# Optimization experiments

Hardware: AMD Instinct MI355X
Metric: run time of the kernel (lower is better)

Reference implementation:

```python
import jax, jax.numpy as jnp
import numpy as np

B, N = 8, 2048
DIN, DH, DE = 32, 64, 64
R = 3          # number_relations
L = 3          # num_layers -> 1 first + 1 block + 1 last
PRED_IN = DH * (L - 1) + DE  # concat: 64*2 + 64 = 192
EPS_BN = 1e-5
EPS_NORM = 1e-12


def setup_inputs() -> dict:
    key = jax.random.key(0)
    ks = jax.random.split(key, 12)
    x = jax.random.normal(ks[0], (B, N, DIN), jnp.float32)
    # relation labels in {0..R}; 0 = no edge, 1..R = relation type
    relation = jax.random.randint(ks[1], (B, N, N), 0, R + 1).astype(jnp.int32)
    # adjacency is the 0/1 edge indicator (float), as the torch code treats it
    adj = (relation > 0).astype(jnp.float32)
    s = 0.05
    w_first = jax.random.normal(ks[2], (R, DIN, DH), jnp.float32) * s
    b_first = jnp.zeros((DH,), jnp.float32)
    w_block = jax.random.normal(ks[3], (R, DH, DH), jnp.float32) * s
    b_block = jnp.zeros((DH,), jnp.float32)
    w_last = jax.random.normal(ks[4], (R, DH, DE), jnp.float32) * s
    b_last = jnp.zeros((DE,), jnp.float32)
    w_map = jax.random.normal(ks[5], (PRED_IN, DE), jnp.float32) * s
    b_map = jnp.zeros((DE,), jnp.float32)
    return {"x": x, "relation": relation, "adj": adj,
            "w_first": w_first, "b_first": b_first,
            "w_block": w_block, "b_block": b_block,
            "w_last": w_last, "b_last": b_last,
            "w_map": w_map, "b_map": b_map}


def _graph_conv(x, rel, W, b):
    # rel: [B,N,N] (int labels or float adjacency); W: [R, din, dout]
    y = jnp.zeros((x.shape[0], x.shape[1], W.shape[2]), x.dtype)
    for i in range(R):  # fixed, small relation count
        mask = (rel == (i + 1)).astype(x.dtype)            # [B,N,N]
        h = jnp.einsum('bij,bjd->bid', mask, x)            # masked aggregation
        y = y + jnp.einsum('bid,de->bie', h, W[i])
    y = y + b
    # F.normalize(p=2, dim=2): v / max(||v||, eps)
    nrm = jnp.sqrt(jnp.sum(y * y, axis=2, keepdims=True))
    return y / jnp.maximum(nrm, EPS_NORM)


def _apply_bn(x):
    # fresh BatchNorm1d(N) in training mode, affine weight=1/bias=0:
    # normalize over (batch, feature) per node index, biased variance
    mean = jnp.mean(x, axis=(0, 2), keepdims=True)
    var = jnp.mean(jnp.square(x - mean), axis=(0, 2), keepdims=True)
    return (x - mean) * jax.lax.rsqrt(var + EPS_BN)


def reference(x, relation, adj, w_first, b_first, w_block, b_block,
              w_last, b_last, w_map, b_map):
    # conv_first uses `relation`
    h = _apply_bn(jax.nn.relu(_graph_conv(x, relation, w_first, b_first)))
    out_all = [jnp.max(h, axis=1)]
    # conv_block and conv_last are (faithfully) called with `adj` as relation
    h = _apply_bn(jax.nn.relu(_graph_conv(h, adj, w_block, b_block)))
    out_all.append(jnp.max(h, axis=1))
    h = _graph_conv(h, adj, w_last, b_last)
    out_all.append(jnp.max(h, axis=1))
    output = jnp.concatenate(out_all, axis=1)        # [B, PRED_IN]
    ypred = output @ w_map + b_map                   # map_model Linear
    return (output, ypred)
```

## Files before the change

kernel.cpp:

```cpp
#include <hip/hip_runtime.h>


#define NN 2048
#define PLANE_W 1048576L

typedef short short8 __attribute__((ext_vector_type(8)));
typedef float floatx4 __attribute__((ext_vector_type(4)));

__device__ __forceinline__ unsigned short f2bf(float x) {
  unsigned u = __float_as_uint(x);
  u += 0x7FFFu + ((u >> 16) & 1u);
  return (unsigned short)(u >> 16);
}

__device__ void dev_xw_first(char* smemc, int u, int tid,
                             const float* __restrict__ x,
                             const float* __restrict__ w,
                             unsigned short* __restrict__ xws) {
  float* xs = (float*)smemc;
  float* wsh = (float*)(smemc + 64 * 33 * 4);
  const int jc = u & 31, b = (u >> 5) & 7, r = u >> 8;
  const int j0 = jc * 64;
  for (int idx = tid; idx < 64 * 32; idx += 256) {
    int row = idx >> 5, f = idx & 31;
    xs[row * 33 + f] = x[((long)b * NN + j0 + row) * 32 + f];
    wsh[idx] = w[r * 2048 + idx];
  }
  __syncthreads();
  const int j = tid & 63, g = tid >> 6;
  const int k = j0 + j;
  const int kblk = k >> 5, kq = (k >> 3) & 3, kj = k & 7;
  unsigned short* dst =
      xws + (((long)(r * 8 + b) * 64 + kblk) * 4 + g) * 512 + kj;
  float xr[32];
#pragma unroll
  for (int f = 0; f < 32; ++f) xr[f] = xs[j * 33 + f];
#pragma unroll
  for (int ii = 0; ii < 16; ++ii) {
    float acc = 0.f;
#pragma unroll
    for (int f = 0; f < 32; ++f) acc += xr[f] * wsh[f * 64 + g * 16 + ii];
    dst[(kq * 16 + ii) * 8] = f2bf(acc);
  }
  __syncthreads();
}

__global__ __launch_bounds__(256) void k_pack_xw1(const int* __restrict__ rel,
                                                  unsigned* __restrict__ planes,
                                                  unsigned* __restrict__ UP,
                                                  const float* __restrict__ x,
                                                  const float* __restrict__ w,
                                                  unsigned short* __restrict__ xws) {
  __shared__ __align__(16) char smem[16640];
  const int bid = blockIdx.x, tid = threadIdx.x;
  if (bid < 768) dev_xw_first(smem, bid, tid, x, w, xws);
  for (long t = (long)bid * 256 + tid; t < 1048576L; t += 4096L * 256) {
    int w32 = (int)(t & 63);
    long bi = t >> 6;
    const int4* rp = (const int4*)(rel + bi * NN + w32 * 32);
    unsigned m0 = 0, m1 = 0, m2 = 0;
#pragma unroll
    for (int c = 0; c < 8; ++c) {
      int4 v = rp[c];
      int vv[4] = {v.x, v.y, v.z, v.w};
#pragma unroll
      for (int j = 0; j < 4; ++j) {
        unsigned b1 = 1u << (c * 4 + j);
        m0 |= (vv[j] == 1) ? b1 : 0u;
        m1 |= (vv[j] == 2) ? b1 : 0u;
        m2 |= (vv[j] == 3) ? b1 : 0u;
      }
    }
    long o = bi * 64 + w32;
    planes[o] = m0;
    planes[PLANE_W + o] = m1;
    planes[2 * PLANE_W + o] = m2;
    UP[o] = m0 | m1 | m2;
  }
}

template <int NREL, bool RELU, bool POOL3>
__global__ __launch_bounds__(512) void k_gemm8(
    const unsigned* __restrict__ planes, const unsigned short* __restrict__ xws,
    const float* __restrict__ bias, float* __restrict__ Hout,
    float* __restrict__ part3) {
  constexpr int SMEM = (NREL * 8448 > 16640) ? NREL * 8448 : 16640;
  __shared__ __align__(16) char smem[SMEM];
  unsigned* mw = (unsigned*)smem;
  floatx4* cb = (floatx4*)smem;
  const int bid = blockIdx.x;
  const int b = bid & 7, it = bid >> 3;
  const int tid = threadIdx.x;
  const int wave = tid >> 6, lane = tid & 63;
  const int m = lane & 15, kq = lane >> 4;
  const int i0 = it * 64;

  floatx4 acc[4][4];
#pragma unroll
  for (int rs = 0; rs < 4; ++rs)
#pragma unroll
    for (int t = 0; t < 4; ++t) acc[rs][t] = floatx4{0, 0, 0, 0};

  for (int chunk = 0; chunk < 2; ++chunk) {
    for (int idx = tid; idx < NREL * 2048; idx += 512) {
      int p = idx >> 11, rem = idx & 2047, row = rem >> 5, w = rem & 31;
      long g = ((long)b * NN + i0 + row) * 64 + chunk * 32 + w;
      unsigned v = (NREL == 3) ? planes[(long)p * PLANE_W + g] : planes[g];
      mw[(p * 64 + row) * 33 + w] = v;
    }
    __syncthreads();
#pragma unroll
    for (int j = 0; j < 4; ++j) {
      const int kk = j * 8 + wave;
      const int kblk = chunk * 32 + kk;
#pragma unroll
      for (int p = 0; p < NREL; ++p) {
        const unsigned short* bb =
            xws + ((long)(p * 8 + b) * 64 + kblk) * 2048 + lane * 8;
        short8 bf0 = *(const short8*)(bb);
        short8 bf1 = *(const short8*)(bb + 512);
        short8 bf2 = *(const short8*)(bb + 1024);
        short8 bf3 = *(const short8*)(bb + 1536);
#pragma unroll
        for (int rs = 0; rs < 4; ++rs) {
          unsigned word = mw[(p * 64 + rs * 16 + m) * 33 + kk];
          unsigned byte = (word >> (kq * 8)) & 0xffu;
          unsigned pp = byte | (byte << 15);
          union {
            unsigned uu[4];
            short8 s8;
          } fr;
          fr.uu[0] = (pp & 0x00010001u) * 0x3F80u;
          fr.uu[1] = (pp & 0x00040004u) * 0x0FE0u;
          fr.uu[2] = (pp & 0x00100010u) * 0x03F8u;
          fr.uu[3] = (pp & 0x00400040u) * 0x00FEu;
          acc[rs][0] = __builtin_amdgcn_mfma_f32_16x16x32_bf16(fr.s8, bf0,
                                                              acc[rs][0], 0, 0, 0);
          acc[rs][1] = __builtin_amdgcn_mfma_f32_16x16x32_bf16(fr.s8, bf1,
                                                              acc[rs][1], 0, 0, 0);
          acc[rs][2] = __builtin_amdgcn_mfma_f32_16x16x32_bf16(fr.s8, bf2,
                                                              acc[rs][2], 0, 0, 0);
          acc[rs][3] = __builtin_amdgcn_mfma_f32_16x16x32_bf16(fr.s8, bf3,
                                                              acc[rs][3], 0, 0, 0);
        }
      }
    }
    __syncthreads();
  }

  for (int k = 7; k >= 1; --k) {
    if (wave == k) {
      if (k == 7) {
#pragma unroll
        for (int rs = 0; rs < 4; ++rs)
#pragma unroll
          for (int t = 0; t < 4; ++t) cb[(rs * 4 + t) * 64 + lane] = acc[rs][t];
      } else {
#pragma unroll
        for (int rs = 0; rs < 4; ++rs)
#pragma unroll
          for (int t = 0; t < 4; ++t) {
            floatx4 v = cb[(rs * 4 + t) * 64 + lane];
            cb[(rs * 4 + t) * 64 + lane] = v + acc[rs][t];
          }
      }
    }
    __syncthreads();
  }
  if (wave == 0) {
#pragma unroll
    for (int rs = 0; rs < 4; ++rs)
#pragma unroll
      for (int t = 0; t < 4; ++t) acc[rs][t] += cb[(rs * 4 + t) * 64 + lane];
    float bv[4];
#pragma unroll
    for (int t = 0; t < 4; ++t) bv[t] = bias[t * 16 + m];
    float pmt[4] = {-3.4e38f, -3.4e38f, -3.4e38f, -3.4e38f};
#pragma unroll
    for (int rs = 0; rs < 4; ++rs) {
      float ss[4];
#pragma unroll
      for (int reg = 0; reg < 4; ++reg) {
#pragma unroll
        for (int t = 0; t < 4; ++t) acc[rs][t][reg] += bv[t];
        ss[reg] = acc[rs][0][reg] * acc[rs][0][reg] +
                  acc[rs][1][reg] * acc[rs][1][reg] +
                  acc[rs][2][reg] * acc[rs][2][reg] +
                  acc[rs][3][reg] * acc[rs][3][reg];
#pragma unroll
        for (int off = 1; off <= 8; off <<= 1)
          ss[reg] += __shfl_xor(ss[reg], off);
        ss[reg] = 1.0f / fmaxf(sqrtf(ss[reg]), 1e-12f);
      }
#pragma unroll
      for (int t = 0; t < 4; ++t) {
#pragma unroll
        for (int reg = 0; reg < 4; ++reg) {
          float o = acc[rs][t][reg] * ss[reg];
          if (RELU) o = fmaxf(o, 0.0f);
          if (POOL3)
            pmt[t] = fmaxf(pmt[t], o);
          else
            Hout[((long)b * NN + i0 + rs * 16 + kq * 4 + reg) * 64 + t * 16 + m] = o;
        }
      }
    }
    if (POOL3) {
#pragma unroll
      for (int t = 0; t < 4; ++t) {
        pmt[t] = fmaxf(pmt[t], __shfl_xor(pmt[t], 16));
        pmt[t] = fmaxf(pmt[t], __shfl_xor(pmt[t], 32));
      }
      if (kq == 0) {
#pragma unroll
        for (int t = 0; t < 4; ++t)
          part3[((long)b * 32 + it) * 64 + t * 16 + m] = pmt[t];
      }
    }
  }
}

__global__ __launch_bounds__(256) void k_xwh_bn(const float* __restrict__ H,
                                                const float* __restrict__ w,
                                                unsigned short* __restrict__ xws,
                                                float* __restrict__ PP) {
  __shared__ float hs[64 * 65];
  __shared__ float wsh[64 * 64];
  __shared__ float sm[64], srs[64];
  const int bid = blockIdx.x, tid = threadIdx.x;
  const int jc = bid & 31, b = bid >> 5;
  const int j0 = jc * 64;
  {
    const int n = tid >> 2, q = tid & 3;
    float s1 = 0.f, s2 = 0.f;
#pragma unroll
    for (int bb = 0; bb < 8; ++bb) {
      const float4* hp =
          (const float4*)(H + ((long)bb * NN + j0 + n) * 64 + q * 16);
#pragma unroll
      for (int c = 0; c < 4; ++c) {
        float4 v = hp[c];
        s1 += v.x + v.y + v.z + v.w;
        s2 += v.x * v.x + v.y * v.y + v.z * v.z + v.w * v.w;
      }
    }
    s1 += __shfl_xor(s1, 1);
    s2 += __shfl_xor(s2, 1);
    s1 += __shfl_xor(s1, 2);
    s2 += __shfl_xor(s2, 2);
    if (q == 0) {
      float mean = s1 * (1.0f / 512.0f);
      float var = fmaxf(s2 * (1.0f / 512.0f) - mean * mean, 0.0f);
      sm[n] = mean;
      srs[n] = rsqrtf(var + 1e-5f);
    }
  }
  __syncthreads();
  for (int idx = tid; idx < 4096; idx += 256) {
    int row = idx >> 6, f = idx & 63;
    float v = H[((long)b * NN + j0 + row) * 64 + f];
    hs[row * 65 + f] = (v - sm[row]) * srs[row];
    wsh[idx] = w[idx];
  }
  __syncthreads();
  {
    const int j = tid & 63, g = tid >> 6;
    const int k = j0 + j;
    const int kblk = k >> 5, kq = (k >> 3) & 3, kj = k & 7;
    unsigned short* dst = xws + (((long)b * 64 + kblk) * 4 + g) * 512 + kj;
    float acc[16];
#pragma unroll
    for (int ii = 0; ii < 16; ++ii) acc[ii] = 0.f;
#pragma unroll
    for (int c = 0; c < 4; ++c) {
      float xr[16];
#pragma unroll
      for (int f = 0; f < 16; ++f) xr[f] = hs[j * 65 + c * 16 + f];
#pragma unroll
      for (int ii = 0; ii < 16; ++ii)
#pragma unroll
        for (int f = 0; f < 16; ++f)
          acc[ii] += xr[f] * wsh[(c * 16 + f) * 64 + g * 16 + ii];
    }
#pragma unroll
    for (int ii = 0; ii < 16; ++ii) dst[(kq * 16 + ii) * 8] = f2bf(acc[ii]);
  }
  if (b == 0) {
#pragma unroll
    for (int part = 0; part < 2; ++part) {
      const int col = part * 256 + tid;
      const int bb = col >> 6, e = col & 63;
      float mx = -3.4e38f;
      for (int n = 0; n < 64; ++n) {
        float v = H[((long)bb * NN + j0 + n) * 64 + e];
        mx = fmaxf(mx, (v - sm[n]) * srs[n]);
      }
      PP[(long)jc * 512 + col] = mx;
    }
  }
}

__global__ __launch_bounds__(512) void k_tail(const float* __restrict__ PP1,
                                              const float* __restrict__ PP2,
                                              const float* __restrict__ P3,
                                              float* __restrict__ out,
                                              const float* __restrict__ wmap,
                                              const float* __restrict__ bmap) {
  const int col = threadIdx.x;
  const int bb = col >> 6, e = col & 63;
  float m1 = -3.4e38f, m2 = -3.4e38f, m3 = -3.4e38f;
#pragma unroll
  for (int c = 0; c < 32; ++c) {
    m1 = fmaxf(m1, PP1[(long)c * 512 + col]);
    m2 = fmaxf(m2, PP2[(long)c * 512 + col]);
    m3 = fmaxf(m3, P3[((long)bb * 32 + c) * 64 + e]);
  }
  out[bb * 192 + e] = m1;
  out[bb * 192 + 64 + e] = m2;
  out[bb * 192 + 128 + e] = m3;
  __syncthreads();
  float acc = bmap[e];
  for (int k = 0; k < 192; ++k) acc += out[bb * 192 + k] * wmap[k * 64 + e];
  out[1536 + bb * 64 + e] = acc;
}

extern "C" void kernel_launch(void* const* d_in, const int* in_sizes, int n_in,
                              void* d_out, int out_size, void* d_ws,
                              size_t ws_size, hipStream_t stream) {
  const float* x = (const float*)d_in[0];
  const int* rel = (const int*)d_in[1];
  const float* w_first = (const float*)d_in[3];
  const float* b_first = (const float*)d_in[4];
  const float* w_block = (const float*)d_in[5];
  const float* b_block = (const float*)d_in[6];
  const float* w_last = (const float*)d_in[7];
  const float* b_last = (const float*)d_in[8];
  const float* w_map = (const float*)d_in[9];
  const float* b_map = (const float*)d_in[10];
  float* out = (float*)d_out;

  char* ws = (char*)d_ws;
  const size_t MB = 1024 * 1024;
  unsigned* PLANES = (unsigned*)(ws);
  unsigned* UP = (unsigned*)(ws + 12 * MB);
  unsigned short* XWS = (unsigned short*)(ws + 16 * MB);
  float* H = (float*)(ws + 24 * MB);
  float* PP1 = (float*)(ws + 28 * MB);
  float* PP2 = (float*)(ws + 29 * MB);
  float* PART3 = (float*)(ws + 30 * MB);

  k_pack_xw1<<<4096, 256, 0, stream>>>(rel, PLANES, UP, x, w_first, XWS);
  k_gemm8<3, true, false><<<256, 512, 0, stream>>>(PLANES, XWS, b_first, H,
                                                   nullptr);
  k_xwh_bn<<<256, 256, 0, stream>>>(H, w_block, XWS, PP1);
  k_gemm8<1, true, false><<<256, 512, 0, stream>>>(UP, XWS, b_block, H,
                                                   nullptr);
  k_xwh_bn<<<256, 256, 0, stream>>>(H, w_last, XWS, PP2);
  k_gemm8<1, false, true><<<256, 512, 0, stream>>>(UP, XWS, b_last, nullptr,
                                                   PART3);
  k_tail<<<1, 512, 0, stream>>>(PP1, PP2, PART3, out, w_map, b_map);
}
```

Before: 356.2 us.

## Fuse relation bitmask packing into first GEMM and tail into last GEMM

The separate pack kernel, which wrote three relation bit-planes to global memory, is removed. The first GEMM kernel now reads the int relation rows directly, builds bitmasks with wave ballots into XOR-swizzled shared memory, and writes only the union plane UP. The final max-pool and linear-map tail is folded into the last GEMM through an atomic counter, so the last-arriving block does that work. This drops the 12MB of plane writes and reads plus one launch, at the cost of a serial rel read inside the GEMM blocks, which now have only 256 blocks of parallelism for the 128MB read.

```diff
diff --git a/kernel.cpp b/kernel.cpp
--- a/kernel.cpp
+++ b/kernel.cpp
@@ -2,7 +2,6 @@
 
 
 #define NN 2048
-#define PLANE_W 1048576L
 
 typedef short short8 __attribute__((ext_vector_type(8)));
 typedef float floatx4 __attribute__((ext_vector_type(4)));
@@ -13,10 +12,108 @@
   return (unsigned short)(u >> 16);
 }
 
-__device__ void dev_xw_first(char* smemc, int u, int tid,
-                             const float* __restrict__ x,
-                             const float* __restrict__ w,
-                             unsigned short* __restrict__ xws) {
+template <bool RELU, bool POOL3>
+__device__ __forceinline__ void gemm_epilogue(
+    floatx4 acc[4][4], char* scratch, const float* __restrict__ bias,
+    float* __restrict__ Hout, float* __restrict__ part3, int b, int it) {
+  const int tid = threadIdx.x;
+  const int wave = tid >> 6, lane = tid & 63;
+  const int m = lane & 15, kq = lane >> 4;
+  const int i0 = it * 64;
+  floatx4* cb = (floatx4*)scratch;
+  for (int k = 7; k >= 1; --k) {
+    if (wave == k) {
+      if (k == 7) {
+#pragma unroll
+        for (int rs = 0; rs < 4; ++rs)
+#pragma unroll
+          for (int t = 0; t < 4; ++t) cb[(rs * 4 + t) * 64 + lane] = acc[rs][t];
+      } else {
+#pragma unroll
+        for (int rs = 0; rs < 4; ++rs)
+#pragma unroll
+          for (int t = 0; t < 4; ++t) {
+            floatx4 v = cb[(rs * 4 + t) * 64 + lane];
+            cb[(rs * 4 + t) * 64 + lane] = v + acc[rs][t];
+          }
+      }
+    }
+    __syncthreads();
+  }
+  if (wave == 0) {
+#pragma unroll
+    for (int rs = 0; rs < 4; ++rs)
+#pragma unroll
+      for (int t = 0; t < 4; ++t) acc[rs][t] += cb[(rs * 4 + t) * 64 + lane];
+    float bv[4];
+#pragma unroll
+    for (int t = 0; t < 4; ++t) bv[t] = bias[t * 16 + m];
+    float pmt[4] = {-3.4e38f, -3.4e38f, -3.4e38f, -3.4e38f};
+#pragma unroll
+    for (int rs = 0; rs < 4; ++rs) {
+      float ss[4];
+#pragma unroll
+      for (int reg = 0; reg < 4; ++reg) {
+#pragma unroll
+        for (int t = 0; t < 4; ++t) acc[rs][t][reg] += bv[t];
+        ss[reg] = acc[rs][0][reg] * acc[rs][0][reg] +
+                  acc[rs][1][reg] * acc[rs][1][reg] +
+                  acc[rs][2][reg] * acc[rs][2][reg] +
+                  acc[rs][3][reg] * acc[rs][3][reg];
+#pragma unroll
+        for (int off = 1; off <= 8; off <<= 1)
+          ss[reg] += __shfl_xor(ss[reg], off);
+        ss[reg] = 1.0f / fmaxf(sqrtf(ss[reg]), 1e-12f);
+      }
+#pragma unroll
+      for (int t = 0; t < 4; ++t) {
+#pragma unroll
+        for (int reg = 0; reg < 4; ++reg) {
+          float o = acc[rs][t][reg] * ss[reg];
+          if (RELU) o = fmaxf(o, 0.0f);
+          if (POOL3)
+            pmt[t] = fmaxf(pmt[t], o);
+          else
+            Hout[((long)b * NN + i0 + rs * 16 + kq * 4 + reg) * 64 + t * 16 + m] = o;
+        }
+      }
+    }
+    if (POOL3) {
+#pragma unroll
+      for (int t = 0; t < 4; ++t) {
+        pmt[t] = fmaxf(pmt[t], __shfl_xor(pmt[t], 16));
+        pmt[t] = fmaxf(pmt[t], __shfl_xor(pmt[t], 32));
+      }
+      if (kq == 0) {
+#pragma unroll
+        for (int t = 0; t < 4; ++t)
+          part3[((long)b * 32 + it) * 64 + t * 16 + m] = pmt[t];
+      }
+    }
+  }
+}
+
+__device__ __forceinline__ short8 expand_frag(unsigned word, int kq) {
+  unsigned byte = (word >> (kq * 8)) & 0xffu;
+  unsigned pp = byte | (byte << 15);
+  union {
+    unsigned uu[4];
+    short8 s8;
+  } fr;
+  fr.uu[0] = (pp & 0x00010001u) * 0x3F80u;
+  fr.uu[1] = (pp & 0x00040004u) * 0x0FE0u;
+  fr.uu[2] = (pp & 0x00100010u) * 0x03F8u;
+  fr.uu[3] = (pp & 0x00400040u) * 0x00FEu;
+  return fr.s8;
+}
+
+__global__ __launch_bounds__(256) void k_xw1(const float* __restrict__ x,
+                                             const float* __restrict__ w,
+                                             unsigned short* __restrict__ xws,
+                                             unsigned* __restrict__ CNT) {
+  __shared__ __align__(16) char smemc[16640];
+  const int u = blockIdx.x, tid = threadIdx.x;
+  if (u == 0 && tid == 0) CNT[0] = 0;
   float* xs = (float*)smemc;
   float* wsh = (float*)(smemc + 64 * 33 * 4);
   const int jc = u & 31, b = (u >> 5) & 7, r = u >> 8;
@@ -42,182 +139,194 @@
     for (int f = 0; f < 32; ++f) acc += xr[f] * wsh[f * 64 + g * 16 + ii];
     dst[(kq * 16 + ii) * 8] = f2bf(acc);
   }
-  __syncthreads();
-}
-
-__global__ __launch_bounds__(256) void k_pack_xw1(const int* __restrict__ rel,
-                                                  unsigned* __restrict__ planes,
-                                                  unsigned* __restrict__ UP,
-                                                  const float* __restrict__ x,
-                                                  const float* __restrict__ w,
-                                                  unsigned short* __restrict__ xws) {
-  __shared__ __align__(16) char smem[16640];
+}
+
+__global__ __launch_bounds__(512) void k_g1(
+    const int* __restrict__ rel, unsigned* __restrict__ UP,
+    const unsigned short* __restrict__ xws, const float* __restrict__ bias,
+    float* __restrict__ Hout) {
+  __shared__ __align__(16) unsigned mw[3 * 4096];
   const int bid = blockIdx.x, tid = threadIdx.x;
-  if (bid < 768) dev_xw_first(smem, bid, tid, x, w, xws);
-  for (long t = (long)bid * 256 + tid; t < 1048576L; t += 4096L * 256) {
-    int w32 = (int)(t & 63);
-    long bi = t >> 6;
-    const int4* rp = (const int4*)(rel + bi * NN + w32 * 32);
-    unsigned m0 = 0, m1 = 0, m2 = 0;
-#pragma unroll
-    for (int c = 0; c < 8; ++c) {
-      int4 v = rp[c];
-      int vv[4] = {v.x, v.y, v.z, v.w};
-#pragma unroll
-      for (int j = 0; j < 4; ++j) {
-        unsigned b1 = 1u << (c * 4 + j);
-        m0 |= (vv[j] == 1) ? b1 : 0u;
-        m1 |= (vv[j] == 2) ? b1 : 0u;
-        m2 |= (vv[j] == 3) ? b1 : 0u;
-      }
-    }
-    long o = bi * 64 + w32;
-    planes[o] = m0;
-    planes[PLANE_W + o] = m1;
-    planes[2 * PLANE_W + o] = m2;
-    UP[o] = m0 | m1 | m2;
-  }
-}
-
-template <int NREL, bool RELU, bool POOL3>
-__global__ __launch_bounds__(512) void k_gemm8(
-    const unsigned* __restrict__ planes, const unsigned short* __restrict__ xws,
-    const float* __restrict__ bias, float* __restrict__ Hout,
-    float* __restrict__ part3) {
-  constexpr int SMEM = (NREL * 8448 > 16640) ? NREL * 8448 : 16640;
-  __shared__ __align__(16) char smem[SMEM];
-  unsigned* mw = (unsigned*)smem;
-  floatx4* cb = (floatx4*)smem;
-  const int bid = blockIdx.x;
   const int b = bid & 7, it = bid >> 3;
-  const int tid = threadIdx.x;
+  const int wave = tid >> 6, lane = tid & 63;
+  const int i0 = it * 64;
+
+  for (int rr = 0; rr < 8; ++rr) {
+    const int row = wave * 8 + rr;
+    const int rsw = row & 31;
+    const long rbase = ((long)b * NN + i0 + row) * NN;
+    for (int jb = 0; jb < 4; ++jb) {
+      int vv[8];
+#pragma unroll
+      for (int u = 0; u < 8; ++u)
+        vv[u] = rel[rbase + (jb * 8 + u) * 64 + lane];
+#pragma unroll
+      for (int u = 0; u < 8; ++u) {
+        const int j = jb * 8 + u;
+        unsigned long long B1 = __ballot(vv[u] == 1);
+        unsigned long long B2 = __ballot(vv[u] == 2);
+        unsigned long long B3 = __ballot(vv[u] == 3);
+        if (lane == 0) {
+          const int o0 = row * 64 + ((2 * j) ^ rsw);
+          const int o1 = row * 64 + ((2 * j + 1) ^ rsw);
+          mw[o0] = (unsigned)B1;
+          mw[o1] = (unsigned)(B1 >> 32);
+          mw[4096 + o0] = (unsigned)B2;
+          mw[4096 + o1] = (unsigned)(B2 >> 32);
+          mw[8192 + o0] = (unsigned)B3;
+          mw[8192 + o1] = (unsigned)(B3 >> 32);
+        }
+      }
+    }
+  }
+  __syncthreads();
+  for (int idx = tid; idx < 4096; idx += 512) {
+    int row = idx >> 6, w = idx & 63, sw = w ^ (row & 31);
+    unsigned uu = mw[row * 64 + sw] | mw[4096 + row * 64 + sw] |
+                  mw[8192 + row * 64 + sw];
+    UP[((long)b * NN + i0 + row) * 64 + w] = uu;
+  }
+
+  const int m = lane & 15, kq = lane >> 4;
+  floatx4 acc[4][4];
+#pragma unroll
+  for (int rs = 0; rs < 4; ++rs)
+#pragma unroll
+    for (int t = 0; t < 4; ++t) acc[rs][t] = floatx4{0, 0, 0, 0};
+
+  for (int kk8 = 0; kk8 < 8; ++kk8) {
+    const int kblk = kk8 * 8 + wave;
+#pragma unroll
+    for (int p = 0; p < 3; ++p) {
+      const unsigned short* bb =
+          xws + ((long)(p * 8 + b) * 64 + kblk) * 2048 + lane * 8;
+      short8 bf0 = *(const short8*)(bb);
+      short8 bf1 = *(const short8*)(bb + 512);
+      short8 bf2 = *(const short8*)(bb + 1024);
+      short8 bf3 = *(const short8*)(bb + 1536);
+#pragma unroll
+      for (int rs = 0; rs < 4; ++rs) {
+        const int row = rs * 16 + m;
+        short8 af = expand_frag(mw[p * 4096 + row * 64 + (kblk ^ (row & 31))], kq);
+        acc[rs][0] = __builtin_amdgcn_mfma_f32_16x16x32_bf16(af, bf0, acc[rs][0], 0, 0, 0);
+        acc[rs][1] = __builtin_amdgcn_mfma_f32_16x16x32_bf16(af, bf1, acc[rs][1], 0, 0, 0);
+        acc[rs][2] = __builtin_amdgcn_mfma_f32_16x16x32_bf16(af, bf2, acc[rs][2], 0, 0, 0);
+        acc[rs][3] = __builtin_amdgcn_mfma_f32_16x16x32_bf16(af, bf3, acc[rs][3], 0, 0, 0);
+      }
+    }
+  }
+  __syncthreads();
+  gemm_epilogue<true, false>(acc, (char*)mw, bias, Hout, nullptr, b, it);
+}
+
+__global__ __launch_bounds__(512) void k_gemm2(
+    const unsigned* __restrict__ UP, const unsigned short* __restrict__ xws,
+    const float* __restrict__ bias, float* __restrict__ Hout) {
+  __shared__ __align__(16) unsigned mw[4096];
+  const int bid = blockIdx.x, tid = threadIdx.x;
+  const int b = bid & 7, it = bid >> 3;
   const int wave = tid >> 6, lane = tid & 63;
   const int m = lane & 15, kq = lane >> 4;
   const int i0 = it * 64;
-
+  for (int idx = tid; idx < 4096; idx += 512) {
+    int row = idx >> 6, w = idx & 63;
+    mw[row * 64 + (w ^ (row & 31))] = UP[((long)b * NN + i0 + row) * 64 + w];
+  }
+  __syncthreads();
   floatx4 acc[4][4];
 #pragma unroll
   for (int rs = 0; rs < 4; ++rs)
 #pragma unroll
     for (int t = 0; t < 4; ++t) acc[rs][t] = floatx4{0, 0, 0, 0};
-
-  for (int chunk = 0; chunk < 2; ++chunk) {
-    for (int idx = tid; idx < NREL * 2048; idx += 512) {
-      int p = idx >> 11, rem = idx & 2047, row = rem >> 5, w = rem & 31;
-      long g = ((long)b * NN + i0 + row) * 64 + chunk * 32 + w;
-      unsigned v = (NREL == 3) ? planes[(long)p * PLANE_W + g] : planes[g];
-      mw[(p * 64 + row) * 33 + w] = v;
-    }
-    __syncthreads();
-#pragma unroll
-    for (int j = 0; j < 4; ++j) {
-      const int kk = j * 8 + wave;
-      const int kblk = chunk * 32 + kk;
-#pragma unroll
-      for (int p = 0; p < NREL; ++p) {
-        const unsigned short* bb =
-            xws + ((long)(p * 8 + b) * 64 + kblk) * 2048 + lane * 8;
-        short8 bf0 = *(const short8*)(bb);
-        short8 bf1 = *(const short8*)(bb + 512);
-        short8 bf2 = *(const short8*)(bb + 1024);
-        short8 bf3 = *(const short8*)(bb + 1536);
-#pragma unroll
-        for (int rs = 0; rs < 4; ++rs) {
-          unsigned word = mw[(p * 64 + rs * 16 + m) * 33 + kk];
-          unsigned byte = (word >> (kq * 8)) & 0xffu;
-          unsigned pp = byte | (byte << 15);
-          union {
-            unsigned uu[4];
-            short8 s8;
-          } fr;
-          fr.uu[0] = (pp & 0x00010001u) * 0x3F80u;
-          fr.uu[1] = (pp & 0x00040004u) * 0x0FE0u;
-          fr.uu[2] = (pp & 0x00100010u) * 0x03F8u;
-          fr.uu[3] = (pp & 0x00400040u) * 0x00FEu;
-          acc[rs][0] = __builtin_amdgcn_mfma_f32_16x16x32_bf16(fr.s8, bf0,
-                                                              acc[rs][0], 0, 0, 0);
-          acc[rs][1] = __builtin_amdgcn_mfma_f32_16x16x32_bf16(fr.s8, bf1,
-                                                              acc[rs][1], 0, 0, 0);
-          acc[rs][2] = __builtin_amdgcn_mfma_f32_16x16x32_bf16(fr.s8, bf2,
-                                                              acc[rs][2], 0, 0, 0);
-          acc[rs][3] = __builtin_amdgcn_mfma_f32_16x16x32_bf16(fr.s8, bf3,
-                                                              acc[rs][3], 0, 0, 0);
-        }
-      }
-    }
-    __syncthreads();
-  }
-
-  for (int k = 7; k >= 1; --k) {
-    if (wave == k) {
-      if (k == 7) {
-#pragma unroll
-        for (int rs = 0; rs < 4; ++rs)
-#pragma unroll
-          for (int t = 0; t < 4; ++t) cb[(rs * 4 + t) * 64 + lane] = acc[rs][t];
-      } else {
-#pragma unroll
-        for (int rs = 0; rs < 4; ++rs)
-#pragma unroll
-          for (int t = 0; t < 4; ++t) {
-            floatx4 v = cb[(rs * 4 + t) * 64 + lane];
-            cb[(rs * 4 + t) * 64 + lane] = v + acc[rs][t];
-          }
-      }
-    }
-    __syncthreads();
-  }
-  if (wave == 0) {
-#pragma unroll
-    for (int rs = 0; rs < 4; ++rs)
-#pragma unroll
-      for (int t = 0; t < 4; ++t) acc[rs][t] += cb[(rs * 4 + t) * 64 + lane];
-    float bv[4];
-#pragma unroll
-    for (int t = 0; t < 4; ++t) bv[t] = bias[t * 16 + m];
-    float pmt[4] = {-3.4e38f, -3.4e38f, -3.4e38f, -3.4e38f};
+  for (int kk8 = 0; kk8 < 8; ++kk8) {
+    const int kblk = kk8 * 8 + wave;
+    const unsigned short* bb = xws + ((long)b * 64 + kblk) * 2048 + lane * 8;
+    short8 bf0 = *(const short8*)(bb);
+    short8 bf1 = *(const short8*)(bb + 512);
+    short8 bf2 = *(const short8*)(bb + 1024);
+    short8 bf3 = *(const short8*)(bb + 1536);
 #pragma unroll
     for (int rs = 0; rs < 4; ++rs) {
-      float ss[4];
-#pragma unroll
-      for (int reg = 0; reg < 4; ++reg) {
-#pragma unroll
-        for (int t = 0; t < 4; ++t) acc[rs][t][reg] += bv[t];
-        ss[reg] = acc[rs][0][reg] * acc[rs][0][reg] +
-                  acc[rs][1][reg] * acc[rs][1][reg] +
-                  acc[rs][2][reg] * acc[rs][2][reg] +
-                  acc[rs][3][reg] * acc[rs][3][reg];
-#pragma unroll
-        for (int off = 1; off <= 8; off <<= 1)
-          ss[reg] += __shfl_xor(ss[reg], off);
-        ss[reg] = 1.0f / fmaxf(sqrtf(ss[reg]), 1e-12f);
-      }
-#pragma unroll
-      for (int t = 0; t < 4; ++t) {
-#pragma unroll
-        for (int reg = 0; reg < 4; ++reg) {
-          float o = acc[rs][t][reg] * ss[reg];
-          if (RELU) o = fmaxf(o, 0.0f);
-          if (POOL3)
-            pmt[t] = fmaxf(pmt[t], o);
-          else
-            Hout[((long)b * NN + i0 + rs * 16 + kq * 4 + reg) * 64 + t * 16 + m] = o;
-        }
-      }
-    }
-    if (POOL3) {
-#pragma unroll
-      for (int t = 0; t < 4; ++t) {
-        pmt[t] = fmaxf(pmt[t], __shfl_xor(pmt[t], 16));
-        pmt[t] = fmaxf(pmt[t], __shfl_xor(pmt[t], 32));
-      }
-      if (kq == 0) {
-#pragma unroll
-        for (int t = 0; t < 4; ++t)
-          part3[((long)b * 32 + it) * 64 + t * 16 + m] = pmt[t];
-      }
-    }
-  }
+      const int row = rs * 16 + m;
+      short8 af = expand_frag(mw[row * 64 + (kblk ^ (row & 31))], kq);
+      acc[rs][0] = __builtin_amdgcn_mfma_f32_16x16x32_bf16(af, bf0, acc[rs][0], 0, 0, 0);
+      acc[rs][1] = __builtin_amdgcn_mfma_f32_16x16x32_bf16(af, bf1, acc[rs][1], 0, 0, 0);
+      acc[rs][2] = __builtin_amdgcn_mfma_f32_16x16x32_bf16(af, bf2, acc[rs][2], 0, 0, 0);
+      acc[rs][3] = __builtin_amdgcn_mfma_f32_16x16x32_bf16(af, bf3, acc[rs][3], 0, 0, 0);
+    }
+  }
+  __syncthreads();
+  gemm_epilogue<true, false>(acc, (char*)mw, bias, Hout, nullptr, b, it);
+}
+
+__global__ __launch_bounds__(512) void k_g3(
+    const unsigned* __restrict__ UP, const unsigned short* __restrict__ xws,
+    const float* __restrict__ bias, float* __restrict__ PART3,
+    const float* __restrict__ PP1, const float* __restrict__ PP2,
+    const float* __restrict__ w_map, const float* __restrict__ b_map,
+    float* __restrict__ out, unsigned* __restrict__ CNT) {
+  __shared__ __align__(16) unsigned mw[4096];
+  __shared__ unsigned lastf;
+  const int bid = blockIdx.x, tid = threadIdx.x;
+  const int b = bid & 7, it = bid >> 3;
+  const int wave = tid >> 6, lane = tid & 63;
+  const int m = lane & 15, kq = lane >> 4;
+  const int i0 = it * 64;
+  for (int idx = tid; idx < 4096; idx += 512) {
+    int row = idx >> 6, w = idx & 63;
+    mw[row * 64 + (w ^ (row & 31))] = UP[((long)b * NN + i0 + row) * 64 + w];
+  }
+  __syncthreads();
+  floatx4 acc[4][4];
+#pragma unroll
+  for (int rs = 0; rs < 4; ++rs)
+#pragma unroll
+    for (int t = 0; t < 4; ++t) acc[rs][t] = floatx4{0, 0, 0, 0};
+  for (int kk8 = 0; kk8 < 8; ++kk8) {
+    const int kblk = kk8 * 8 + wave;
+    const unsigned short* bb = xws + ((long)b * 64 + kblk) * 2048 + lane * 8;
+    short8 bf0 = *(const short8*)(bb);
+    short8 bf1 = *(const short8*)(bb + 512);
+    short8 bf2 = *(const short8*)(bb + 1024);
+    short8 bf3 = *(const short8*)(bb + 1536);
+#pragma unroll
+    for (int rs = 0; rs < 4; ++rs) {
+      const int row = rs * 16 + m;
+      short8 af = expand_frag(mw[row * 64 + (kblk ^ (row & 31))], kq);
+      acc[rs][0] = __builtin_amdgcn_mfma_f32_16x16x32_bf16(af, bf0, acc[rs][0], 0, 0, 0);
+      acc[rs][1] = __builtin_amdgcn_mfma_f32_16x16x32_bf16(af, bf1, acc[rs][1], 0, 0, 0);
+      acc[rs][2] = __builtin_amdgcn_mfma_f32_16x16x32_bf16(af, bf2, acc[rs][2], 0, 0, 0);
+      acc[rs][3] = __builtin_amdgcn_mfma_f32_16x16x32_bf16(af, bf3, acc[rs][3], 0, 0, 0);
+    }
+  }
+  __syncthreads();
+  gemm_epilogue<false, true>(acc, (char*)mw, bias, nullptr, PART3, b, it);
+
+  __threadfence();
+  __syncthreads();
+  if (tid == 0) {
+    unsigned r = __hip_atomic_fetch_add(CNT, 1u, __ATOMIC_ACQ_REL,
+                                        __HIP_MEMORY_SCOPE_AGENT);
+    lastf = (r == 255u) ? 1u : 0u;
+  }
+  __syncthreads();
+  if (!lastf) return;
+  __threadfence();
+  const int bb = tid >> 6, e = tid & 63;
+  float m1 = -3.4e38f, m2 = -3.4e38f, m3 = -3.4e38f;
+#pragma unroll
+  for (int c = 0; c < 32; ++c) {
+    m1 = fmaxf(m1, PP1[(long)c * 512 + tid]);
+    m2 = fmaxf(m2, PP2[(long)c * 512 + tid]);
+    m3 = fmaxf(m3, PART3[((long)bb * 32 + c) * 64 + e]);
+  }
+  out[bb * 192 + e] = m1;
+  out[bb * 192 + 64 + e] = m2;
+  out[bb * 192 + 128 + e] = m3;
+  __syncthreads();
+  float a = b_map[e];
+  for (int k = 0; k < 192; ++k) a += out[bb * 192 + k] * w_map[k * 64 + e];
+  out[1536 + bb * 64 + e] = a;
 }
 
 __global__ __launch_bounds__(256) void k_xwh_bn(const float* __restrict__ H,
@@ -298,30 +407,6 @@
       PP[(long)jc * 512 + col] = mx;
     }
   }
-}
-
-__global__ __launch_bounds__(512) void k_tail(const float* __restrict__ PP1,
-                                              const float* __restrict__ PP2,
-                                              const float* __restrict__ P3,
-                                              float* __restrict__ out,
-                                              const float* __restrict__ wmap,
-                                              const float* __restrict__ bmap) {
-  const int col = threadIdx.x;
-  const int bb = col >> 6, e = col & 63;
-  float m1 = -3.4e38f, m2 = -3.4e38f, m3 = -3.4e38f;
-#pragma unroll
-  for (int c = 0; c < 32; ++c) {
-    m1 = fmaxf(m1, PP1[(long)c * 512 + col]);
-    m2 = fmaxf(m2, PP2[(long)c * 512 + col]);
-    m3 = fmaxf(m3, P3[((long)bb * 32 + c) * 64 + e]);
-  }
-  out[bb * 192 + e] = m1;
-  out[bb * 192 + 64 + e] = m2;
-  out[bb * 192 + 128 + e] = m3;
-  __syncthreads();
-  float acc = bmap[e];
-  for (int k = 0; k < 192; ++k) acc += out[bb * 192 + k] * wmap[k * 64 + e];
-  out[1536 + bb * 64 + e] = acc;
 }
 
 extern "C" void kernel_launch(void* const* d_in, const int* in_sizes, int n_in,
@@ -341,22 +426,19 @@
 
   char* ws = (char*)d_ws;
   const size_t MB = 1024 * 1024;
-  unsigned* PLANES = (unsigned*)(ws);
-  unsigned* UP = (unsigned*)(ws + 12 * MB);
-  unsigned short* XWS = (unsigned short*)(ws + 16 * MB);
-  float* H = (float*)(ws + 24 * MB);
-  float* PP1 = (float*)(ws + 28 * MB);
-  float* PP2 = (float*)(ws + 29 * MB);
-  float* PART3 = (float*)(ws + 30 * MB);
-
-  k_pack_xw1<<<4096, 256, 0, stream>>>(rel, PLANES, UP, x, w_first, XWS);
-  k_gemm8<3, true, false><<<256, 512, 0, stream>>>(PLANES, XWS, b_first, H,
-                                                   nullptr);
+  unsigned* UP = (unsigned*)(ws);
+  unsigned short* XWS = (unsigned short*)(ws + 4 * MB);
+  float* H = (float*)(ws + 12 * MB);
+  float* PP1 = (float*)(ws + 16 * MB);
+  float* PP2 = (float*)(ws + 17 * MB);
+  float* PART3 = (float*)(ws + 18 * MB);
+  unsigned* CNT = (unsigned*)(ws + 19 * MB);
+
+  k_xw1<<<768, 256, 0, stream>>>(x, w_first, XWS, CNT);
+  k_g1<<<256, 512, 0, stream>>>(rel, UP, XWS, b_first, H);
   k_xwh_bn<<<256, 256, 0, stream>>>(H, w_block, XWS, PP1);
-  k_gemm8<1, true, false><<<256, 512, 0, stream>>>(UP, XWS, b_block, H,
-                                                   nullptr);
+  k_gemm2<<<256, 512, 0, stream>>>(UP, XWS, b_block, H);
   k_xwh_bn<<<256, 256, 0, stream>>>(H, w_last, XWS, PP2);
-  k_gemm8<1, false, true><<<256, 512, 0, stream>>>(UP, XWS, b_last, nullptr,
-                                                   PART3);
-  k_tail<<<1, 512, 0, stream>>>(PP1, PP2, PART3, out, w_map, b_map);
-}
+  k_g3<<<256, 512, 0, stream>>>(UP, XWS, b_last, PART3, PP1, PP2, w_map,
+                                b_map, out, CNT);
+}
```

After: 385.3 us. +8.2%, slower.
